# Optimization experiments

Measured on AMD Instinct MI355X. Metric: run time of the kernel, lower is better.

The kernel has to match this reference:

```python
import jax, jax.numpy as jnp
import numpy as np

TOK, B, DIM, TXT, NT, KS, H = 576, 64, 1024, 512, 1000, 3, 24
SCALE = TXT ** -0.5  # qk_scale = head_dim**-0.5 with head_dim = out_dim = 512


def _layernorm(x, g, b, eps=1e-5):
    m = jnp.mean(x, axis=-1, keepdims=True)
    v = jnp.var(x, axis=-1, keepdims=True)
    return (x - m) * jax.lax.rsqrt(v + eps) * g + b


def _cross_attn(q_in, kv, Wq):
    # q_in: [B,tok,DIM] -> q: [B,tok,TXT]; kv: [B,NT,TXT] serves as both K and V
    q = jnp.einsum('btd,de->bte', q_in, Wq)
    attn = jax.nn.softmax(jnp.einsum('bte,bne->btn', q, kv) * SCALE, axis=-1)
    return jnp.einsum('btn,bne->bte', attn, kv)


def _dwconv(z, w):
    # z: [B,1,H,H], w: [1,1,KS,KS], padding KS//2, stride 1
    return jax.lax.conv_general_dilated(
        z, w, window_strides=(1, 1), padding=((KS // 2, KS // 2), (KS // 2, KS // 2)),
        dimension_numbers=('NCHW', 'OIHW', 'NCHW'))


def setup_inputs() -> dict:
    key = jax.random.key(0)
    ks = jax.random.split(key, 6)
    return {
        'x': jax.random.normal(ks[0], (TOK + 1, B, DIM), jnp.float32),
        'text_fea': jax.random.normal(ks[1], (NT, B, TXT), jnp.float32),
        'ln_q1_g': jnp.ones((DIM,), jnp.float32), 'ln_q1_b': jnp.zeros((DIM,), jnp.float32),
        'ln_q2_g': jnp.ones((DIM,), jnp.float32), 'ln_q2_b': jnp.zeros((DIM,), jnp.float32),
        'ln_kv_g': jnp.ones((TXT,), jnp.float32), 'ln_kv_b': jnp.zeros((TXT,), jnp.float32),
        'Wq1': jax.random.normal(ks[2], (DIM, TXT), jnp.float32) * 0.02,
        'Wq2': jax.random.normal(ks[3], (DIM, TXT), jnp.float32) * 0.02,
        'conv_dw': jax.random.normal(ks[4], (1, 1, KS, KS), jnp.float32) * 0.1,
        'conv_final': jax.random.normal(ks[5], (DIM, TXT), jnp.float32) * 0.02,  # [out,in]
    }


def reference(x, text_fea, ln_q1_g, ln_q1_b, ln_q2_g, ln_q2_b, ln_kv_g, ln_kv_b,
              Wq1, Wq2, conv_dw, conv_final):
    x_cls, xp = x[:1], x[1:]                      # [1,B,DIM], [TOK,B,DIM]
    x_loc = jnp.transpose(xp, (1, 0, 2))          # [B,TOK,DIM]
    kv = _layernorm(jnp.transpose(text_fea, (1, 0, 2)), ln_kv_g, ln_kv_b)  # [B,NT,TXT]

    o1 = _cross_attn(_layernorm(x_loc, ln_q1_g, ln_q1_b), kv, Wq1)  # [B,TOK,TXT]
    o2 = _cross_attn(_layernorm(x_loc, ln_q2_g, ln_q2_b), kv, Wq2)

    x1 = jnp.transpose(o1, (0, 2, 1)).reshape(B, TXT, H, H)
    x2 = jnp.transpose(o2, (0, 2, 1)).reshape(B, TXT, H, H)

    avg_x = jnp.mean(x1, axis=1, keepdims=True)   # [B,1,H,H]
    max_x = jnp.max(x2, axis=1, keepdims=True)
    gate1 = jax.nn.sigmoid(_dwconv(avg_x, conv_dw))
    gate2 = jax.nn.sigmoid(_dwconv(max_x, conv_dw))

    x_se = x1 * gate1 + x2 * gate2                # [B,TXT,H,H]
    y = jnp.einsum('bchw,oc->bohw', x_se, conv_final)  # 1x1 conv, padding 0

    y = jnp.transpose(y.reshape(B, DIM, TOK), (2, 0, 1))  # [TOK,B,DIM]
    return jnp.concatenate([x_cls, y], axis=0)
```

## Files before the change

### kernel.cpp

```cpp
#include <hip/hip_runtime.h>

#define B_    64
#define TOK_  576
#define DIM_  1024
#define TXT_  512
#define NT_   1000
#define NTQ_  1024
#define NTP_  1024
#define H_    24
#define BT_   (B_ * TOK_)
static constexpr float SCALE_ = 0.0441941738241592f;

typedef __bf16 bf16x8 __attribute__((ext_vector_type(8)));
typedef float  f32x4  __attribute__((ext_vector_type(4)));

__device__ __forceinline__ unsigned short f2bf(float f) {
    unsigned u = __float_as_uint(f);
    u += 0x7fffu + ((u >> 16) & 1u);
    return (unsigned short)(u >> 16);
}
__device__ __forceinline__ float bf2f(unsigned short h) {
    return __uint_as_float(((unsigned)h) << 16);
}
__device__ __forceinline__ f32x4 mfma16(bf16x8 a, bf16x8 b, f32x4 c) {
    return __builtin_amdgcn_mfma_f32_16x16x32_bf16(a, b, c, 0, 0, 0);
}
__device__ __forceinline__ void unpack8(uint4 v, float* f) {
    unsigned a0 = v.x, a1 = v.y, a2 = v.z, a3 = v.w;
    f[0] = bf2f((unsigned short)(a0 & 0xffff)); f[1] = bf2f((unsigned short)(a0 >> 16));
    f[2] = bf2f((unsigned short)(a1 & 0xffff)); f[3] = bf2f((unsigned short)(a1 >> 16));
    f[4] = bf2f((unsigned short)(a2 & 0xffff)); f[5] = bf2f((unsigned short)(a2 >> 16));
    f[6] = bf2f((unsigned short)(a3 & 0xffff)); f[7] = bf2f((unsigned short)(a3 >> 16));
}
__device__ __forceinline__ unsigned encmax(float f) {
    unsigned u = __float_as_uint(f);
    return (u & 0x80000000u) ? ~u : (u | 0x80000000u);
}
__device__ __forceinline__ float decmax(unsigned k) {
    unsigned u = (k & 0x80000000u) ? (k ^ 0x80000000u) : ~k;
    return __uint_as_float(u);
}

typedef const __attribute__((address_space(1))) unsigned int* as1_u32p;
typedef __attribute__((address_space(3))) unsigned int* as3_u32p;
__device__ __forceinline__ void gll16(const void* g, void* l) {
    __builtin_amdgcn_global_load_lds((as1_u32p)g, (as3_u32p)l, 16, 0, 0);
}

__global__ void k_prep(const float* __restrict__ wq1, const float* __restrict__ wq2,
                       const float* __restrict__ g1, const float* __restrict__ g2,
                       const float* __restrict__ b1, const float* __restrict__ b2,
                       const float* __restrict__ wf,
                       unsigned short* __restrict__ wqt, float* __restrict__ qbias,
                       unsigned short* __restrict__ wfb, float* __restrict__ stats) {
    __shared__ float tile[64][68];
    int bx = blockIdx.x, t = threadIdx.x;
    if (bx < 256) {
        int br = bx >> 7, kt = (bx >> 3) & 15, nt = bx & 7;
        const float* wq = br ? wq2 : wq1;
        const float* gg = br ? g2 : g1;
#pragma unroll
        for (int i = 0; i < 4; ++i) {
            int idx4 = t + i * 256;
            int kl = idx4 >> 4, n4 = (idx4 & 15) * 4;
            float gv = gg[kt * 64 + kl];
            float4 v = *reinterpret_cast<const float4*>(wq + (size_t)(kt * 64 + kl) * 512 + nt * 64 + n4);
            tile[kl][n4 + 0] = v.x * gv; tile[kl][n4 + 1] = v.y * gv;
            tile[kl][n4 + 2] = v.z * gv; tile[kl][n4 + 3] = v.w * gv;
        }
        __syncthreads();
#pragma unroll
        for (int i = 0; i < 4; ++i) {
            int idx4 = t + i * 256;
            int nl = idx4 >> 4, k4 = (idx4 & 15) * 4;
            ushort4 o = make_ushort4(f2bf(tile[k4 + 0][nl]), f2bf(tile[k4 + 1][nl]),
                                     f2bf(tile[k4 + 2][nl]), f2bf(tile[k4 + 3][nl]));
            *reinterpret_cast<ushort4*>(wqt + (size_t)br * 512 * 1024 + (size_t)(nt * 64 + nl) * 1024 + kt * 64 + k4) = o;
        }
    } else if (bx < 272) {
        int bb2 = bx - 256;
        int br = bb2 >> 3, e0 = (bb2 & 7) * 64;
        int e = e0 + (t & 63), part = t >> 6;
        const float* wq = br ? wq2 : wq1;
        const float* bb = br ? b2 : b1;
        float s = 0.f;
        for (int d = part * 256; d < part * 256 + 256; ++d) s += bb[d] * wq[(size_t)d * 512 + e];
        float* red = &tile[0][0];
        red[t] = s;
        __syncthreads();
        if (t < 64) qbias[br * 512 + e0 + t] = red[t] + red[64 + t] + red[128 + t] + red[192 + t];
    } else if (bx < 784) {
        int i = (bx - 272) * 256 + t;
        float4 v = *reinterpret_cast<const float4*>(wf + (size_t)i * 4);
        ushort4 o = make_ushort4(f2bf(v.x), f2bf(v.y), f2bf(v.z), f2bf(v.w));
        *reinterpret_cast<ushort4*>(wfb + (size_t)i * 4) = o;
    } else {
        int i = (bx - 784) * 256 + t;
        *reinterpret_cast<float4*>(stats + (size_t)i * 4) = make_float4(0.f, 0.f, 0.f, 0.f);
    }
}

__global__ __launch_bounds__(512, 4) void k_lnorm(const float* __restrict__ tf,
                                                  const float* __restrict__ g,
                                                  const float* __restrict__ bta,
                                                  const float* __restrict__ x,
                                                  unsigned short* __restrict__ kvn,
                                                  unsigned short* __restrict__ xn) {
    int bid = blockIdx.x;
    int l = threadIdx.x & 63;
    if (bid < 8192) {
        int trow = bid * 8 + (threadIdx.x >> 6);
        int n = trow >> 6, b = trow & 63;
        unsigned short* dst = kvn + ((size_t)b * NTQ_ + n) * TXT_;
        if (n >= NT_) {
            *reinterpret_cast<ushort4*>(dst + l * 4) = make_ushort4(0, 0, 0, 0);
            *reinterpret_cast<ushort4*>(dst + 256 + l * 4) = make_ushort4(0, 0, 0, 0);
            return;
        }
        const float* src = tf + (size_t)trow * TXT_;
        float4 v0 = *reinterpret_cast<const float4*>(src + l * 4);
        float4 v1 = *reinterpret_cast<const float4*>(src + 256 + l * 4);
        float s  = v0.x + v0.y + v0.z + v0.w + v1.x + v1.y + v1.z + v1.w;
        float ss = v0.x * v0.x + v0.y * v0.y + v0.z * v0.z + v0.w * v0.w
                 + v1.x * v1.x + v1.y * v1.y + v1.z * v1.z + v1.w * v1.w;
#pragma unroll
        for (int d = 1; d < 64; d <<= 1) { s += __shfl_xor(s, d); ss += __shfl_xor(ss, d); }
        float m = s * (1.f / TXT_);
        float rs = rsqrtf(ss * (1.f / TXT_) - m * m + 1e-5f);
        float4 g0 = *reinterpret_cast<const float4*>(g + l * 4);
        float4 g1 = *reinterpret_cast<const float4*>(g + 256 + l * 4);
        float4 b0 = *reinterpret_cast<const float4*>(bta + l * 4);
        float4 b1 = *reinterpret_cast<const float4*>(bta + 256 + l * 4);
        ushort4 o0 = make_ushort4(f2bf((v0.x - m) * rs * g0.x + b0.x),
                                  f2bf((v0.y - m) * rs * g0.y + b0.y),
                                  f2bf((v0.z - m) * rs * g0.z + b0.z),
                                  f2bf((v0.w - m) * rs * g0.w + b0.w));
        ushort4 o1 = make_ushort4(f2bf((v1.x - m) * rs * g1.x + b1.x),
                                  f2bf((v1.y - m) * rs * g1.y + b1.y),
                                  f2bf((v1.z - m) * rs * g1.z + b1.z),
                                  f2bf((v1.w - m) * rs * g1.w + b1.w));
        *reinterpret_cast<ushort4*>(dst + l * 4) = o0;
        *reinterpret_cast<ushort4*>(dst + 256 + l * 4) = o1;
    } else {
        int gr = 64 + (bid - 8192) * 8 + (threadIdx.x >> 6);
        int b = gr & 63, tk = (gr >> 6) - 1;
        const float* src = x + (size_t)gr * DIM_;
        float4 v[4];
#pragma unroll
        for (int j = 0; j < 4; ++j) v[j] = *reinterpret_cast<const float4*>(src + j * 256 + l * 4);
        float s = 0.f, ss = 0.f;
#pragma unroll
        for (int j = 0; j < 4; ++j) {
            s += v[j].x + v[j].y + v[j].z + v[j].w;
            ss += v[j].x * v[j].x + v[j].y * v[j].y + v[j].z * v[j].z + v[j].w * v[j].w;
        }
#pragma unroll
        for (int d = 1; d < 64; d <<= 1) { s += __shfl_xor(s, d); ss += __shfl_xor(ss, d); }
        float m = s * (1.f / DIM_);
        float rs = rsqrtf(ss * (1.f / DIM_) - m * m + 1e-5f);
        unsigned short* dst = xn + ((size_t)b * TOK_ + tk) * DIM_;
#pragma unroll
        for (int j = 0; j < 4; ++j) {
            ushort4 o = make_ushort4(f2bf((v[j].x - m) * rs), f2bf((v[j].y - m) * rs),
                                     f2bf((v[j].z - m) * rs), f2bf((v[j].w - m) * rs));
            *reinterpret_cast<ushort4*>(dst + j * 256 + l * 4) = o;
        }
    }
}

__global__ void k_kvt(const unsigned short* __restrict__ kvn, unsigned short* __restrict__ kvt) {
    __shared__ unsigned short tile[64][68];
    int bx = blockIdx.x;
    int b = bx >> 7, rem = bx & 127, et = rem >> 4, nt = rem & 15;
    int t = threadIdx.x;
#pragma unroll
    for (int i = 0; i < 4; ++i) {
        int idx4 = t + i * 256;
        int nl = idx4 >> 4, e4 = (idx4 & 15) * 4;
        int ng = nt * 64 + nl;
        ushort4 v = make_ushort4(0, 0, 0, 0);
        if (ng < NT_) v = *reinterpret_cast<const ushort4*>(kvn + ((size_t)b * NTQ_ + ng) * TXT_ + et * 64 + e4);
        tile[nl][e4 + 0] = v.x; tile[nl][e4 + 1] = v.y; tile[nl][e4 + 2] = v.z; tile[nl][e4 + 3] = v.w;
    }
    __syncthreads();
#pragma unroll
    for (int i = 0; i < 4; ++i) {
        int idx4 = t + i * 256;
        int el = idx4 >> 4, n4 = (idx4 & 15) * 4;
        ushort4 o = make_ushort4(tile[n4 + 0][el], tile[n4 + 1][el], tile[n4 + 2][el], tile[n4 + 3][el]);
        *reinterpret_cast<ushort4*>(kvt + ((size_t)b * TXT_ + et * 64 + el) * NTP_ + nt * 64 + n4) = o;
    }
}

__device__ __forceinline__ void gemm_loop_gll(const unsigned short* __restrict__ A,
                                              const unsigned short* __restrict__ Bp,
                                              int K, unsigned short* a_lds, unsigned short* b_lds,
                                              int tid, f32x4 acc[4][4]) {
    const int l = tid & 63, w = tid >> 6;
    const int l16 = l & 15, lg = l >> 4;
    const int wm = w & 1, wn = w >> 1;
    const f32x4 fz = {0.f, 0.f, 0.f, 0.f};
#pragma unroll
    for (int mt = 0; mt < 4; ++mt)
#pragma unroll
        for (int nt = 0; nt < 4; ++nt) acc[mt][nt] = fz;
    const int lrow = l >> 3;
    const int k8g = (l & 7) ^ lrow;
    const int nk = K >> 6;
    for (int kt = 0; kt < nk; ++kt) {
#pragma unroll
        for (int i = 0; i < 4; ++i) {
            int row = i * 32 + w * 8 + lrow;
            gll16(A + (size_t)row * K + kt * 64 + k8g * 8, &a_lds[(i * 256 + w * 64) * 8]);
        }
#pragma unroll
        for (int i = 0; i < 4; ++i) {
            int row = i * 32 + w * 8 + lrow;
            gll16(Bp + (size_t)row * K + kt * 64 + k8g * 8, &b_lds[(i * 256 + w * 64) * 8]);
        }
        __syncthreads();
#pragma unroll
        for (int kk = 0; kk < 2; ++kk) {
            bf16x8 af[4], bff[4];
#pragma unroll
            for (int mt = 0; mt < 4; ++mt) {
                int row = wm * 64 + mt * 16 + l16;
                int gs = (kk * 4 + lg) ^ (row & 7);
                af[mt] = *reinterpret_cast<const bf16x8*>(a_lds + row * 64 + gs * 8);
            }
#pragma unroll
            for (int nt = 0; nt < 4; ++nt) {
                int row = wn * 64 + nt * 16 + l16;
                int gs = (kk * 4 + lg) ^ (row & 7);
                bff[nt] = *reinterpret_cast<const bf16x8*>(b_lds + row * 64 + gs * 8);
            }
#pragma unroll
            for (int mt = 0; mt < 4; ++mt)
#pragma unroll
                for (int nt = 0; nt < 4; ++nt)
                    acc[mt][nt] = mfma16(af[mt], bff[nt], acc[mt][nt]);
        }
        __syncthreads();
    }
}

__device__ __forceinline__ void gemm_loop96(const unsigned short* __restrict__ A,
                                            const unsigned short* __restrict__ Bp,
                                            int K, unsigned short* a_lds, unsigned short* b_lds,
                                            int tid, f32x4 acc[3][4]) {
    const int l = tid & 63, w = tid >> 6;
    const int l16 = l & 15, lg = l >> 4;
    const int wm = w & 1, wn = w >> 1;
    const f32x4 fz = {0.f, 0.f, 0.f, 0.f};
#pragma unroll
    for (int mt = 0; mt < 3; ++mt)
#pragma unroll
        for (int nt = 0; nt < 4; ++nt) acc[mt][nt] = fz;
    const int lrow = l >> 3;
    const int k8g = (l & 7) ^ lrow;
    const int nk = K >> 6;
    for (int kt = 0; kt < nk; ++kt) {
#pragma unroll
        for (int i = 0; i < 3; ++i) {
            int row = i * 32 + w * 8 + lrow;
            gll16(A + (size_t)row * K + kt * 64 + k8g * 8, &a_lds[(i * 256 + w * 64) * 8]);
        }
#pragma unroll
        for (int i = 0; i < 4; ++i) {
            int row = i * 32 + w * 8 + lrow;
            gll16(Bp + (size_t)row * K + kt * 64 + k8g * 8, &b_lds[(i * 256 + w * 64) * 8]);
        }
        __syncthreads();
#pragma unroll
        for (int kk = 0; kk < 2; ++kk) {
            bf16x8 af[3], bff[4];
#pragma unroll
            for (int mt = 0; mt < 3; ++mt) {
                int row = wm * 48 + mt * 16 + l16;
                int gs = (kk * 4 + lg) ^ (row & 7);
                af[mt] = *reinterpret_cast<const bf16x8*>(a_lds + row * 64 + gs * 8);
            }
#pragma unroll
            for (int nt = 0; nt < 4; ++nt) {
                int row = wn * 64 + nt * 16 + l16;
                int gs = (kk * 4 + lg) ^ (row & 7);
                bff[nt] = *reinterpret_cast<const bf16x8*>(b_lds + row * 64 + gs * 8);
            }
#pragma unroll
            for (int mt = 0; mt < 3; ++mt)
#pragma unroll
                for (int nt = 0; nt < 4; ++nt)
                    acc[mt][nt] = mfma16(af[mt], bff[nt], acc[mt][nt]);
        }
        __syncthreads();
    }
}

__global__ __launch_bounds__(256, 4) void k_qgemm(const unsigned short* __restrict__ xn,
                                                  const unsigned short* __restrict__ wqt,
                                                  const float* __restrict__ qbias,
                                                  unsigned short* __restrict__ qb) {
    int bid = blockIdx.x;
    int vb = (bid & 7) * 288 + (bid >> 3);
    int bn = vb & 3;
    int t = vb >> 2;
    int br = (t >= 288) ? 1 : 0;
    int bm = t - br * 288;
    const unsigned short* A = xn + (size_t)bm * 128 * DIM_;
    const unsigned short* Bp = wqt + (size_t)br * 512 * 1024 + (size_t)bn * 128 * 1024;
    unsigned short* C = qb + (size_t)br * BT_ * TXT_;
    const float* bias = qbias + br * 512;
    __shared__ unsigned short a_lds[128 * 64];
    __shared__ unsigned short b_lds[128 * 64];
    f32x4 acc[4][4];
    gemm_loop_gll(A, Bp, DIM_, a_lds, b_lds, threadIdx.x, acc);
    const int l = threadIdx.x & 63, w = threadIdx.x >> 6;
    const int l16 = l & 15, lg = l >> 4, wm = w & 1, wn = w >> 1;
#pragma unroll
    for (int mt = 0; mt < 4; ++mt)
#pragma unroll
        for (int nt = 0; nt < 4; ++nt) {
            int col = bn * 128 + wn * 64 + nt * 16 + l16;
            float bv = bias[col];
#pragma unroll
            for (int r = 0; r < 4; ++r) {
                int row = bm * 128 + wm * 64 + mt * 16 + lg * 4 + r;
                C[(size_t)row * TXT_ + col] = f2bf((acc[mt][nt][r] + bv) * SCALE_);
            }
        }
}

__global__ __launch_bounds__(256, 4) void k_score(const unsigned short* __restrict__ qbuf,
                                                  const unsigned short* __restrict__ kvn,
                                                  unsigned short* __restrict__ P,
                                                  float* __restrict__ denom, int br) {
    int bid = blockIdx.x;
    int vb = (bid & 7) * 384 + (bid >> 3);
    int tile = vb % 48, b = vb / 48;
    int mt = tile >> 3, nt = tile & 7;
    const unsigned short* A = qbuf + ((size_t)br * BT_ + (size_t)b * TOK_ + mt * 96) * TXT_;
    const unsigned short* Bp = kvn + (size_t)b * NTQ_ * TXT_ + (size_t)nt * 128 * TXT_;
    __shared__ unsigned short a_lds[96 * 64];
    __shared__ unsigned short b_lds[128 * 64];
    f32x4 acc[3][4];
    gemm_loop96(A, Bp, TXT_, a_lds, b_lds, threadIdx.x, acc);
    const int l = threadIdx.x & 63, w = threadIdx.x >> 6;
    const int l16 = l & 15, lg = l >> 4, wm = w & 1, wn = w >> 1;
    float* dn = denom + (size_t)br * BT_;
#pragma unroll
    for (int mt2 = 0; mt2 < 3; ++mt2)
#pragma unroll
        for (int r = 0; r < 4; ++r) {
            int row = b * TOK_ + mt * 96 + wm * 48 + mt2 * 16 + lg * 4 + r;
            float s = 0.f;
#pragma unroll
            for (int nt2 = 0; nt2 < 4; ++nt2) {
                int col = nt * 128 + wn * 64 + nt2 * 16 + l16;
                float p = (col < NT_) ? __expf(acc[mt2][nt2][r]) : 0.f;
                s += p;
                P[(size_t)row * NTP_ + col] = f2bf(p);
            }
#pragma unroll
            for (int d = 1; d < 16; d <<= 1) s += __shfl_xor(s, d);
            if (l16 == 0) atomicAdd(&dn[row], s);
        }
}

__global__ __launch_bounds__(256, 4) void k_pv(const unsigned short* __restrict__ P,
                                               const unsigned short* __restrict__ kvt,
                                               const float* __restrict__ denom,
                                               unsigned short* __restrict__ ob,
                                               float* __restrict__ avgs,
                                               unsigned* __restrict__ maxe, int br) {
    int bid = blockIdx.x;
    int vb = (bid & 7) * 192 + (bid >> 3);
    int tile = vb % 24, b = vb / 24;
    int mt = tile >> 2, nt = tile & 3;
    const unsigned short* A = P + ((size_t)b * TOK_ + mt * 96) * NTP_;
    const unsigned short* Bp = kvt + (size_t)b * TXT_ * NTP_ + (size_t)nt * 128 * NTP_;
    __shared__ unsigned short a_lds[96 * 64];
    __shared__ unsigned short b_lds[128 * 64];
    f32x4 acc[3][4];
    gemm_loop96(A, Bp, NTP_, a_lds, b_lds, threadIdx.x, acc);
    const int l = threadIdx.x & 63, w = threadIdx.x >> 6;
    const int l16 = l & 15, lg = l >> 4, wm = w & 1, wn = w >> 1;
    const float* dn = denom + (size_t)br * BT_;
#pragma unroll
    for (int mt2 = 0; mt2 < 3; ++mt2)
#pragma unroll
        for (int r = 0; r < 4; ++r) {
            int row = b * TOK_ + mt * 96 + wm * 48 + mt2 * 16 + lg * 4 + r;
            float inv = 1.f / dn[row];
            unsigned short* dst = ob + ((size_t)br * BT_ + row) * TXT_;
            float sum = 0.f, mx = -1e30f;
#pragma unroll
            for (int nt2 = 0; nt2 < 4; ++nt2) {
                int col = nt * 128 + wn * 64 + nt2 * 16 + l16;
                float o = acc[mt2][nt2][r] * inv;
                dst[col] = f2bf(o);
                sum += o;
                mx = fmaxf(mx, o);
            }
#pragma unroll
            for (int d = 1; d < 16; d <<= 1) {
                sum += __shfl_xor(sum, d);
                mx = fmaxf(mx, __shfl_xor(mx, d));
            }
            if (l16 == 0) {
                if (br == 0) atomicAdd(&avgs[row], sum);
                else         atomicMax(&maxe[row], encmax(mx));
            }
        }
}

__global__ __launch_bounds__(256, 4) void k_fgemm(const unsigned short* __restrict__ xse,
                                                  const unsigned short* __restrict__ wfb,
                                                  float* __restrict__ out) {
    int bid = blockIdx.x;
    int vb = (bid & 7) * 288 + (bid >> 3);
    int bn = vb & 7, bm = vb >> 3;
    const unsigned short* A = xse + (size_t)bm * 128 * TXT_;
    const unsigned short* Bp = wfb + (size_t)bn * 128 * TXT_;
    __shared__ unsigned short a_lds[128 * 64];
    __shared__ unsigned short b_lds[128 * 64];
    f32x4 acc[4][4];
    gemm_loop_gll(A, Bp, TXT_, a_lds, b_lds, threadIdx.x, acc);
    const int l = threadIdx.x & 63, w = threadIdx.x >> 6;
    const int l16 = l & 15, lg = l >> 4, wm = w & 1, wn = w >> 1;
#pragma unroll
    for (int mt = 0; mt < 4; ++mt)
#pragma unroll
        for (int r = 0; r < 4; ++r) {
            int rowg = bm * 128 + wm * 64 + mt * 16 + lg * 4 + r;
            int b = rowg / TOK_, tk = rowg - b * TOK_;
            float* dst = out + ((size_t)(tk + 1) * B_ + b) * DIM_;
#pragma unroll
            for (int nt = 0; nt < 4; ++nt) {
                int col = bn * 128 + wn * 64 + nt * 16 + l16;
                dst[col] = acc[mt][nt][r];
            }
        }
}

__global__ void k_xse(const unsigned short* __restrict__ o1, const unsigned short* __restrict__ o2,
                      const float* __restrict__ avgs, const unsigned* __restrict__ maxe,
                      const float* __restrict__ cdw, unsigned short* __restrict__ xse) {
    int idx8 = blockIdx.x * 256 + threadIdx.x;
    int bt = idx8 >> 6, e8 = threadIdx.x & 63;
    float gg1 = 0.f, gg2 = 0.f;
    if (e8 == 0) {
        int b = bt / TOK_, hw = bt - b * TOK_, h = hw / H_, ww = hw - h * H_;
        float a1 = 0.f, a2 = 0.f;
#pragma unroll
        for (int ky = 0; ky < 3; ++ky)
#pragma unroll
            for (int kx = 0; kx < 3; ++kx) {
                int hh = h + ky - 1, wx = ww + kx - 1;
                if (hh >= 0 && hh < H_ && wx >= 0 && wx < H_) {
                    float wv = cdw[ky * 3 + kx];
                    int s = b * TOK_ + hh * H_ + wx;
                    a1 += wv * avgs[s] * (1.f / TXT_);
                    a2 += wv * decmax(maxe[s]);
                }
            }
        gg1 = 1.f / (1.f + __expf(-a1));
        gg2 = 1.f / (1.f + __expf(-a2));
    }
    gg1 = __shfl(gg1, 0);
    gg2 = __shfl(gg2, 0);
    float f1[8], f2[8];
    unpack8(*reinterpret_cast<const uint4*>(o1 + (size_t)bt * TXT_ + e8 * 8), f1);
    unpack8(*reinterpret_cast<const uint4*>(o2 + (size_t)bt * TXT_ + e8 * 8), f2);
    unsigned r[4];
#pragma unroll
    for (int j = 0; j < 4; ++j) {
        unsigned lo = f2bf(f1[2 * j] * gg1 + f2[2 * j] * gg2);
        unsigned hi = f2bf(f1[2 * j + 1] * gg1 + f2[2 * j + 1] * gg2);
        r[j] = lo | (hi << 16);
    }
    uint4 o = make_uint4(r[0], r[1], r[2], r[3]);
    *reinterpret_cast<uint4*>(xse + (size_t)bt * TXT_ + e8 * 8) = o;
}

extern "C" void kernel_launch(void* const* d_in, const int* in_sizes, int n_in,
                              void* d_out, int out_size, void* d_ws, size_t ws_size,
                              hipStream_t stream) {
    (void)in_sizes; (void)n_in; (void)out_size; (void)ws_size;
    const float* x    = (const float*)d_in[0];
    const float* tf   = (const float*)d_in[1];
    const float* lq1g = (const float*)d_in[2];
    const float* lq1b = (const float*)d_in[3];
    const float* lq2g = (const float*)d_in[4];
    const float* lq2b = (const float*)d_in[5];
    const float* lkvg = (const float*)d_in[6];
    const float* lkvb = (const float*)d_in[7];
    const float* wq1  = (const float*)d_in[8];
    const float* wq2  = (const float*)d_in[9];
    const float* cdw  = (const float*)d_in[10];
    const float* wf   = (const float*)d_in[11];
    float* out = (float*)d_out;

    char* ws = (char*)d_ws;
    size_t off = 0;
    auto carve = [&](size_t bytes) { char* p = ws + off; off += (bytes + 255) & ~(size_t)255; return p; };
    unsigned short* kvn  = (unsigned short*)carve((size_t)B_ * NTQ_ * TXT_ * 2);
    unsigned short* kvt  = (unsigned short*)carve((size_t)B_ * TXT_ * NTP_ * 2);
    unsigned short* wqt  = (unsigned short*)carve((size_t)2 * 512 * 1024 * 2);
    unsigned short* wfb  = (unsigned short*)carve((size_t)1024 * 512 * 2);
    float* qbias = (float*)carve((size_t)2 * 512 * 4);
    float* stats = (float*)carve((size_t)4 * BT_ * 4);
    float* denom = stats;
    float* avgs  = stats + 2 * BT_;
    unsigned* maxe = (unsigned*)(stats + 3 * BT_);
    unsigned short* xn   = (unsigned short*)carve((size_t)BT_ * DIM_ * 2);
    unsigned short* qbuf = (unsigned short*)carve((size_t)2 * BT_ * TXT_ * 2);
    unsigned short* ob   = (unsigned short*)carve((size_t)2 * BT_ * TXT_ * 2);
    unsigned short* Pm   = xn;
    unsigned short* xse  = qbuf;

    hipMemcpyAsync(out, x, (size_t)B_ * DIM_ * sizeof(float), hipMemcpyDeviceToDevice, stream);

    k_prep<<<928, 256, 0, stream>>>(wq1, wq2, lq1g, lq2g, lq1b, lq2b, wf, wqt, qbias, wfb, stats);
    k_lnorm<<<12800, 512, 0, stream>>>(tf, lkvg, lkvb, x, kvn, xn);
    k_kvt<<<8192, 256, 0, stream>>>(kvn, kvt);
    k_qgemm<<<2304, 256, 0, stream>>>(xn, wqt, qbias, qbuf);
    k_score<<<3072, 256, 0, stream>>>(qbuf, kvn, Pm, denom, 0);
    k_pv<<<1536, 256, 0, stream>>>(Pm, kvt, denom, ob, avgs, maxe, 0);
    k_score<<<3072, 256, 0, stream>>>(qbuf, kvn, Pm, denom, 1);
    k_pv<<<1536, 256, 0, stream>>>(Pm, kvt, denom, ob, avgs, maxe, 1);
    k_xse<<<9216, 256, 0, stream>>>(ob, ob + (size_t)BT_ * TXT_, avgs, maxe, cdw, xse);
    k_fgemm<<<2304, 256, 0, stream>>>(xse, wfb, out);
}
```

Before: 615.0 us.

## Replace Q projection GEMM with 256x256-tile 8-wave double-buffered pipelined kernel

The 128x128-tile Q-projection GEMM is replaced by a 512-thread kernel that computes 256x256 output tiles, covering both query branches in one pass over A. K-tiles are split into half-planes, and the next tile is prefetched into alternate LDS planes with explicit vmcnt waits and barriers. MFMA bursts are raised to higher scheduling priority. The aim is less redundant A/B traffic and load latency hidden behind matrix math, at the cost of 128KB of LDS, more registers per thread and a hand-tuned barrier schedule that is fragile.

```diff
diff --git a/kernel.cpp b/kernel.cpp
--- a/kernel.cpp
+++ b/kernel.cpp
@@ -13,6 +13,9 @@
 
 typedef __bf16 bf16x8 __attribute__((ext_vector_type(8)));
 typedef float  f32x4  __attribute__((ext_vector_type(4)));
+
+#define SBAR()  asm volatile("s_barrier" ::: "memory")
+#define VMC(N)  asm volatile("s_waitcnt vmcnt(" #N ")" ::: "memory")
 
 __device__ __forceinline__ unsigned short f2bf(float f) {
     unsigned u = __float_as_uint(f);
@@ -192,6 +195,114 @@
     }
 }
 
+__global__ __launch_bounds__(512, 2) void k_qgemm8(const unsigned short* __restrict__ xn,
+                                                   const unsigned short* __restrict__ wqt,
+                                                   const float* __restrict__ qbias,
+                                                   unsigned short* __restrict__ qb) {
+    __shared__ unsigned short lds[8][8192];
+    int bid = blockIdx.x;
+    int vb = (bid & 7) * 72 + (bid >> 3);
+    int bn = vb & 3, bm = vb >> 2;
+    const unsigned short* Ab = xn + (size_t)bm * 256 * DIM_;
+    const unsigned short* Bb = wqt + (size_t)bn * 256 * DIM_;
+    const int tid = threadIdx.x, w = tid >> 6, l = tid & 63;
+    const int l16 = l & 15, lg = l >> 4;
+    const int wm = w >> 2, wn = w & 3;
+    const int srow = l >> 2;
+    const int sgs = (l & 3) ^ ((srow >> 1) & 3);
+
+    auto STAGE = [&](int plane, const unsigned short* src, int kt, int kh) {
+#pragma unroll
+        for (int i = 0; i < 2; ++i) {
+            int row = i * 128 + w * 16 + srow;
+            gll16(src + (size_t)row * DIM_ + kt * 64 + kh * 32 + sgs * 8,
+                  &lds[plane][(i * 128 + w * 16) * 32]);
+        }
+    };
+    auto RD = [&](int plane, int row) -> bf16x8 {
+        int gg = lg ^ ((row >> 1) & 3);
+        return *reinterpret_cast<const bf16x8*>(&lds[plane][row * 32 + gg * 8]);
+    };
+
+    const f32x4 fz = {0.f, 0.f, 0.f, 0.f};
+    f32x4 acc[8][4];
+#pragma unroll
+    for (int mt = 0; mt < 8; ++mt)
+#pragma unroll
+        for (int nt = 0; nt < 4; ++nt) acc[mt][nt] = fz;
+
+    const int NK = DIM_ / 64;
+    STAGE(0, Ab, 0, 0); STAGE(2, Bb, 0, 0); STAGE(1, Ab, 0, 1); STAGE(3, Bb, 0, 1);
+
+    bf16x8 af_[4], bf_[4];
+    for (int kt = 0; kt < NK; ++kt) {
+        const int pb = (kt & 1) * 4, nb = pb ^ 4;
+        const bool pf = (kt + 1 < NK);
+        if (pf) { STAGE(nb + 0, Ab, kt + 1, 0); VMC(6); } else { VMC(4); }
+        SBAR();
+#pragma unroll
+        for (int nt = 0; nt < 4; ++nt) bf_[nt] = RD(pb + 2, wn * 64 + nt * 16 + l16);
+#pragma unroll
+        for (int mt = 0; mt < 4; ++mt) af_[mt] = RD(pb + 0, wm * 128 + mt * 16 + l16);
+        __builtin_amdgcn_s_setprio(1);
+#pragma unroll
+        for (int mt = 0; mt < 4; ++mt)
+#pragma unroll
+            for (int nt = 0; nt < 4; ++nt) acc[mt][nt] = mfma16(af_[mt], bf_[nt], acc[mt][nt]);
+        __builtin_amdgcn_s_setprio(0);
+        SBAR();
+        if (pf) STAGE(nb + 2, Bb, kt + 1, 0);
+        SBAR();
+#pragma unroll
+        for (int mt = 0; mt < 4; ++mt) af_[mt] = RD(pb + 0, wm * 128 + 64 + mt * 16 + l16);
+        __builtin_amdgcn_s_setprio(1);
+#pragma unroll
+        for (int mt = 0; mt < 4; ++mt)
+#pragma unroll
+            for (int nt = 0; nt < 4; ++nt) acc[4 + mt][nt] = mfma16(af_[mt], bf_[nt], acc[4 + mt][nt]);
+        __builtin_amdgcn_s_setprio(0);
+        SBAR();
+        if (pf) { STAGE(nb + 1, Ab, kt + 1, 1); VMC(6); } else { VMC(0); }
+        SBAR();
+#pragma unroll
+        for (int nt = 0; nt < 4; ++nt) bf_[nt] = RD(pb + 3, wn * 64 + nt * 16 + l16);
+#pragma unroll
+        for (int mt = 0; mt < 4; ++mt) af_[mt] = RD(pb + 1, wm * 128 + mt * 16 + l16);
+        __builtin_amdgcn_s_setprio(1);
+#pragma unroll
+        for (int mt = 0; mt < 4; ++mt)
+#pragma unroll
+            for (int nt = 0; nt < 4; ++nt) acc[mt][nt] = mfma16(af_[mt], bf_[nt], acc[mt][nt]);
+        __builtin_amdgcn_s_setprio(0);
+        SBAR();
+        if (pf) STAGE(nb + 3, Bb, kt + 1, 1);
+        SBAR();
+#pragma unroll
+        for (int mt = 0; mt < 4; ++mt) af_[mt] = RD(pb + 1, wm * 128 + 64 + mt * 16 + l16);
+        __builtin_amdgcn_s_setprio(1);
+#pragma unroll
+        for (int mt = 0; mt < 4; ++mt)
+#pragma unroll
+            for (int nt = 0; nt < 4; ++nt) acc[4 + mt][nt] = mfma16(af_[mt], bf_[nt], acc[4 + mt][nt]);
+        __builtin_amdgcn_s_setprio(0);
+        SBAR();
+    }
+#pragma unroll
+    for (int mt = 0; mt < 8; ++mt)
+#pragma unroll
+        for (int nt = 0; nt < 4; ++nt) {
+            int colg = bn * 256 + wn * 64 + nt * 16 + l16;
+            int br = colg >> 9, col = colg & 511;
+            float bv = qbias[colg];
+            unsigned short* C = qb + (size_t)br * BT_ * TXT_;
+#pragma unroll
+            for (int r = 0; r < 4; ++r) {
+                int row = bm * 256 + wm * 128 + mt * 16 + lg * 4 + r;
+                C[(size_t)row * TXT_ + col] = f2bf((acc[mt][nt][r] + bv) * SCALE_);
+            }
+        }
+}
+
 __device__ __forceinline__ void gemm_loop_gll(const unsigned short* __restrict__ A,
                                               const unsigned short* __restrict__ Bp,
                                               int K, unsigned short* a_lds, unsigned short* b_lds,
@@ -294,40 +405,6 @@
         }
         __syncthreads();
     }
-}
-
-__global__ __launch_bounds__(256, 4) void k_qgemm(const unsigned short* __restrict__ xn,
-                                                  const unsigned short* __restrict__ wqt,
-                                                  const float* __restrict__ qbias,
-                                                  unsigned short* __restrict__ qb) {
-    int bid = blockIdx.x;
-    int vb = (bid & 7) * 288 + (bid >> 3);
-    int bn = vb & 3;
-    int t = vb >> 2;
-    int br = (t >= 288) ? 1 : 0;
-    int bm = t - br * 288;
-    const unsigned short* A = xn + (size_t)bm * 128 * DIM_;
-    const unsigned short* Bp = wqt + (size_t)br * 512 * 1024 + (size_t)bn * 128 * 1024;
-    unsigned short* C = qb + (size_t)br * BT_ * TXT_;
-    const float* bias = qbias + br * 512;
-    __shared__ unsigned short a_lds[128 * 64];
-    __shared__ unsigned short b_lds[128 * 64];
-    f32x4 acc[4][4];
-    gemm_loop_gll(A, Bp, DIM_, a_lds, b_lds, threadIdx.x, acc);
-    const int l = threadIdx.x & 63, w = threadIdx.x >> 6;
-    const int l16 = l & 15, lg = l >> 4, wm = w & 1, wn = w >> 1;
-#pragma unroll
-    for (int mt = 0; mt < 4; ++mt)
-#pragma unroll
-        for (int nt = 0; nt < 4; ++nt) {
-            int col = bn * 128 + wn * 64 + nt * 16 + l16;
-            float bv = bias[col];
-#pragma unroll
-            for (int r = 0; r < 4; ++r) {
-                int row = bm * 128 + wm * 64 + mt * 16 + lg * 4 + r;
-                C[(size_t)row * TXT_ + col] = f2bf((acc[mt][nt][r] + bv) * SCALE_);
-            }
-        }
 }
 
 __global__ __launch_bounds__(256, 4) void k_score(const unsigned short* __restrict__ qbuf,
@@ -523,7 +600,7 @@
     k_prep<<<928, 256, 0, stream>>>(wq1, wq2, lq1g, lq2g, lq1b, lq2b, wf, wqt, qbias, wfb, stats);
     k_lnorm<<<12800, 512, 0, stream>>>(tf, lkvg, lkvb, x, kvn, xn);
     k_kvt<<<8192, 256, 0, stream>>>(kvn, kvt);
-    k_qgemm<<<2304, 256, 0, stream>>>(xn, wqt, qbias, qbuf);
+    k_qgemm8<<<576, 512, 0, stream>>>(xn, wqt, qbias, qbuf);
     k_score<<<3072, 256, 0, stream>>>(qbuf, kvn, Pm, denom, 0);
     k_pv<<<1536, 256, 0, stream>>>(Pm, kvt, denom, ob, avgs, maxe, 0);
     k_score<<<3072, 256, 0, stream>>>(qbuf, kvn, Pm, denom, 1);
```

Result: slower. 632.4 us (+2.8%).
